# Kernel tuning notes

Measured on AMD Instinct MI355X. Metric: run time of the kernel, lower is better.

## Reference

```python
import jax, jax.numpy as jnp
import numpy as np

B, S, D = 8, 2048, 512
LN_EPS = 1e-5

def _layernorm(x, gamma, beta):
    mu = jnp.mean(x, axis=-1, keepdims=True)
    var = jnp.mean(jnp.square(x - mu), axis=-1, keepdims=True)
    return (x - mu) * jax.lax.rsqrt(var + LN_EPS) * gamma + beta

def setup_inputs() -> dict:
    key = jax.random.key(0)
    ks = jax.random.split(key, 10)
    s_in = 1.0 / np.sqrt(2 * D)
    s_d = 1.0 / np.sqrt(D)
    return {
        "Noise_x": jax.random.normal(ks[0], (B, S, D), jnp.float32),
        "X": jax.random.normal(ks[1], (B, S, D), jnp.float32),
        "cond": jax.random.normal(ks[2], (B, S, D), jnp.float32),
        "W_gate": jax.random.normal(ks[3], (2 * D, D), jnp.float32) * s_in,
        "b_gate": jnp.zeros((D,), jnp.float32),
        "W1": jax.random.normal(ks[4], (D, 2 * D), jnp.float32) * s_d,
        "b1": jnp.zeros((2 * D,), jnp.float32),
        "W2": jax.random.normal(ks[5], (2 * D, D), jnp.float32) * s_in,
        "b2": jnp.zeros((D,), jnp.float32),
        "g1": jnp.ones((D,), jnp.float32),
        "be1": jnp.zeros((D,), jnp.float32),
        "g2": jnp.ones((D,), jnp.float32),
        "be2": jnp.zeros((D,), jnp.float32),
    }

def reference(Noise_x, X, cond, W_gate, b_gate, W1, b1, W2, b2, g1, be1, g2, be2):
    # gated fusion of noise and condition
    combined = jnp.concatenate([Noise_x, cond], axis=-1)            # [B,S,2D]
    gate = jax.nn.sigmoid(combined @ W_gate + b_gate)               # [B,S,D]
    fused = gate * Noise_x + (1.0 - gate) * cond                    # [B,S,D]
    # hand-rolled attention: Q = fused, K = V = X
    scale = 1.0 / jnp.sqrt(jnp.asarray(D, fused.dtype))
    scores = jnp.einsum('bqd,bkd->bqk', fused, X) * scale           # [B,S,S]
    attn = jax.nn.softmax(scores, axis=-1)
    attn_out = jnp.einsum('bqk,bkd->bqd', attn, X)                  # [B,S,D]
    # residual + norm, FFN (exact GELU as in torch default), residual + norm
    q = _layernorm(fused + attn_out, g1, be1)
    ff = jax.nn.gelu(q @ W1 + b1, approximate=False) @ W2 + b2
    return _layernorm(q + ff, g2, be2)
```

## Files before the change

### kernel.cpp

```cpp
#include <hip/hip_runtime.h>
#include <math.h>

typedef unsigned short ushort_t;
typedef unsigned int uint_t;
typedef __attribute__((ext_vector_type(8))) short short8;
typedef __attribute__((ext_vector_type(4))) float floatx4;

constexpr int B = 8;
constexpr int S = 2048;
constexpr int D = 512;
constexpr int BS = B * S;
constexpr float LN_EPS = 1e-5f;
constexpr float ATTN_SCALE = 0.04419417382415922f;


__device__ __forceinline__ ushort_t f2bf(float f) {
    union { float f; uint_t u; } x; x.f = f;
    uint_t r = x.u + 0x7fffu + ((x.u >> 16) & 1u);
    return (ushort_t)(r >> 16);
}
__device__ __forceinline__ float bf2f(ushort_t h) {
    union { uint_t u; float f; } y; y.u = ((uint_t)h) << 16;
    return y.f;
}
__device__ __forceinline__ short8 pack8(float4 a, float4 b) {
    short8 p;
    p[0] = (short)f2bf(a.x); p[1] = (short)f2bf(a.y);
    p[2] = (short)f2bf(a.z); p[3] = (short)f2bf(a.w);
    p[4] = (short)f2bf(b.x); p[5] = (short)f2bf(b.y);
    p[6] = (short)f2bf(b.z); p[7] = (short)f2bf(b.w);
    return p;
}

#define SWZ_DECODE(bx, by, bz)                                                 \
    int bx, by, bz;                                                            \
    {                                                                          \
        const int gx = gridDim.x, gy = gridDim.y;                              \
        const int nwg = gx * gy * (int)gridDim.z;                              \
        const int F = blockIdx.x + gx * (blockIdx.y + gy * blockIdx.z);        \
        const int L = (F & 7) * (nwg >> 3) + (F >> 3);                         \
        bx = L % gx;                                                           \
        const int l2 = L / gx;                                                 \
        by = l2 % gy;                                                          \
        bz = l2 / gy;                                                          \
    }

__device__ __forceinline__ float blk_reduce_sum(float v, float* sm) {
#pragma unroll
    for (int o = 32; o; o >>= 1) v += __shfl_down(v, o, 64);
    __syncthreads();
    if ((threadIdx.x & 63) == 0) sm[threadIdx.x >> 6] = v;
    __syncthreads();
    return sm[0] + sm[1] + sm[2] + sm[3];
}
__device__ __forceinline__ float blk_reduce_max(float v, float* sm) {
#pragma unroll
    for (int o = 32; o; o >>= 1) v = fmaxf(v, __shfl_down(v, o, 64));
    __syncthreads();
    if ((threadIdx.x & 63) == 0) sm[threadIdx.x >> 6] = v;
    __syncthreads();
    return fmaxf(fmaxf(sm[0], sm[1]), fmaxf(sm[2], sm[3]));
}

__global__ __launch_bounds__(256) void transpose_cvt(
    const float* __restrict__ in, ushort_t* __restrict__ out, int R, int C,
    ushort_t* __restrict__ out2) {
    __shared__ float tl[32][33];
    const size_t zoff = (size_t)blockIdx.z * R * C;
    const int tx = threadIdx.x & 31, ty = threadIdx.x >> 5;
    const int c0 = blockIdx.x * 32, r0 = blockIdx.y * 32;
#pragma unroll
    for (int i = 0; i < 4; i++) {
        const float v = in[zoff + (size_t)(r0 + ty + i * 8) * C + c0 + tx];
        tl[ty + i * 8][tx] = v;
        if (out2) out2[zoff + (size_t)(r0 + ty + i * 8) * C + c0 + tx] = f2bf(v);
    }
    __syncthreads();
#pragma unroll
    for (int i = 0; i < 4; i++)
        out[zoff + (size_t)(c0 + ty + i * 8) * R + r0 + tx] = f2bf(tl[tx][ty + i * 8]);
}

#define IDX512()                                                               \
    const int t = threadIdx.x;                                                 \
    const int srow = t >> 2;                                       \
    const int scol = (t & 3) * 8;                               \
    const int lane = t & 63, w = t >> 6;                           \
    const int wm = (w >> 2) * 64, wn = (w & 3) * 32;                           \
    const int fr = lane & 15, fq = lane >> 4;

#define MFMA8W(Asp, Bsp)                                                       \
    {                                                                          \
        short8 af[4], bfg[2];                                                  \
        _Pragma("unroll") for (int i = 0; i < 4; i++)                          \
            af[i]  = *(const short8*)&(Asp)[(wm + i * 16 + fr) * 40 + fq * 8]; \
        _Pragma("unroll") for (int j = 0; j < 2; j++)                          \
            bfg[j] = *(const short8*)&(Bsp)[(wn + j * 16 + fr) * 40 + fq * 8]; \
        _Pragma("unroll") for (int i = 0; i < 4; i++)                          \
            _Pragma("unroll") for (int j = 0; j < 2; j++)                      \
                acc[i][j] = __builtin_amdgcn_mfma_f32_16x16x32_bf16(           \
                    af[i], bfg[j], acc[i][j], 0, 0, 0);                        \
    }

__global__ __launch_bounds__(512) void gate_gemm(
    const float* __restrict__ NX, const float* __restrict__ CD,
    const ushort_t* __restrict__ WgT, const float* __restrict__ bg,
    ushort_t* __restrict__ Fb) {
    __shared__ ushort_t As[2][128 * 40];
    __shared__ ushort_t Bs[2][128 * 40];
    SWZ_DECODE(bx, by, bz);
    (void)bz;
    IDX512();
    const int m0 = by * 128, n0 = bx * 128;
    floatx4 acc[4][2];
#pragma unroll
    for (int i = 0; i < 4; i++)
#pragma unroll
        for (int j = 0; j < 2; j++) {
            acc[i][j][0] = 0.f; acc[i][j][1] = 0.f;
            acc[i][j][2] = 0.f; acc[i][j][3] = 0.f;
        }
    const ushort_t* Bb = WgT + (size_t)n0 * 1024;

    float4 fa0, fa1;
    int4 b0;
    {
        const float* p0 = NX + (size_t)(m0 + srow) * 512 + scol;
        fa0 = *(const float4*)p0;  fa1 = *(const float4*)(p0 + 4);
        b0 = *(const int4*)(Bb + (size_t)srow * 1024 + scol);
        *(short8*)&As[0][srow * 40 + scol] = pack8(fa0, fa1);
        *(int4*)&Bs[0][srow * 40 + scol] = b0;
    }
    {
        const float* p0 = NX + (size_t)(m0 + srow) * 512 + 32 + scol;
        fa0 = *(const float4*)p0;  fa1 = *(const float4*)(p0 + 4);
        b0 = *(const int4*)(Bb + (size_t)srow * 1024 + 32 + scol);
    }
    __syncthreads();

    int cur = 0;
    for (int k0 = 0; k0 < 1024; k0 += 32) {
        MFMA8W(As[cur], Bs[cur]);
        const int kn = k0 + 32;
        if (kn < 1024) {
            *(short8*)&As[cur ^ 1][srow * 40 + scol] = pack8(fa0, fa1);
            *(int4*)&Bs[cur ^ 1][srow * 40 + scol] = b0;
            const int kf = kn + 32;
            if (kf < 1024) {
                const float* Asrc = (kf < 512) ? NX : CD;
                const int kk = kf & 511;
                const float* p0 = Asrc + (size_t)(m0 + srow) * 512 + kk + scol;
                fa0 = *(const float4*)p0;  fa1 = *(const float4*)(p0 + 4);
                b0 = *(const int4*)(Bb + (size_t)srow * 1024 + kf + scol);
            }
        }
        __syncthreads();
        cur ^= 1;
    }

#pragma unroll
    for (int i = 0; i < 4; i++) {
#pragma unroll
        for (int j = 0; j < 2; j++) {
#pragma unroll
            for (int r = 0; r < 4; r++) {
                const int m = m0 + wm + i * 16 + fq * 4 + r;
                const int n = n0 + wn + j * 16 + fr;
                const float z = acc[i][j][r] + bg[n];
                const float g = 1.f / (1.f + expf(-z));
                const size_t idx = (size_t)m * 512 + n;
                Fb[idx] = f2bf(g * NX[idx] + (1.f - g) * CD[idx]);
            }
        }
    }
}

template <int EPI>
__global__ __launch_bounds__(512) void gemm2_std(
    const ushort_t* __restrict__ A, int lda, long sAz,
    const ushort_t* __restrict__ Bt, int ldb, long sBz,
    void* __restrict__ Cv, int ldc, long sCz,
    int K, const float* __restrict__ bias, float scale, int init) {
    __shared__ ushort_t As[2][128 * 40];
    __shared__ ushort_t Bs[2][128 * 40];
    SWZ_DECODE(bx, by, bz);
    IDX512();
    const int m0 = by * 128, n0 = bx * 128;
    floatx4 acc[4][2];
#pragma unroll
    for (int i = 0; i < 4; i++)
#pragma unroll
        for (int j = 0; j < 2; j++) {
            acc[i][j][0] = 0.f; acc[i][j][1] = 0.f;
            acc[i][j][2] = 0.f; acc[i][j][3] = 0.f;
        }
    const ushort_t* Ab = A + (size_t)bz * sAz + (size_t)m0 * lda;
    const ushort_t* Bb = Bt + (size_t)bz * sBz + (size_t)n0 * ldb;

    int4 a0 = *(const int4*)(Ab + (size_t)srow * lda + scol);
    int4 b0 = *(const int4*)(Bb + (size_t)srow * ldb + scol);
    *(int4*)&As[0][srow * 40 + scol] = a0;
    *(int4*)&Bs[0][srow * 40 + scol] = b0;
    if (32 < K) {
        a0 = *(const int4*)(Ab + (size_t)srow * lda + 32 + scol);
        b0 = *(const int4*)(Bb + (size_t)srow * ldb + 32 + scol);
    }
    __syncthreads();

    int cur = 0;
    for (int k0 = 0; k0 < K; k0 += 32) {
        MFMA8W(As[cur], Bs[cur]);
        const int kn = k0 + 32;
        if (kn < K) {
            *(int4*)&As[cur ^ 1][srow * 40 + scol] = a0;
            *(int4*)&Bs[cur ^ 1][srow * 40 + scol] = b0;
            const int kf = kn + 32;
            if (kf < K) {
                a0 = *(const int4*)(Ab + (size_t)srow * lda + kf + scol);
                b0 = *(const int4*)(Bb + (size_t)srow * ldb + kf + scol);
            }
        }
        __syncthreads();
        cur ^= 1;
    }

#pragma unroll
    for (int i = 0; i < 4; i++) {
#pragma unroll
        for (int j = 0; j < 2; j++) {
#pragma unroll
            for (int r = 0; r < 4; r++) {
                const int m = m0 + wm + i * 16 + fq * 4 + r;
                const int n = n0 + wn + j * 16 + fr;
                float v = acc[i][j][r];
                if (EPI == 0) {
                    ushort_t* C = (ushort_t*)Cv + (size_t)bz * sCz;
                    C[(size_t)m * ldc + n] = f2bf(v * scale);
                } else if (EPI == 1) {
                    const float x = v + bias[n];
                    const float gl = 0.5f * x * (1.f + erff(x * 0.70710678118654752f));
                    ushort_t* C = (ushort_t*)Cv;
                    C[(size_t)m * ldc + n] = f2bf(gl);
                } else {
                    float* T = (float*)Cv;
                    const size_t idx = (size_t)m * ldc + n;
                    T[idx] = T[idx] + v + (init ? bias[n] : 0.f);
                }
            }
        }
    }
}

#define IDX128()                                                               \
    const int t = threadIdx.x;                                                 \
    const int sr = t >> 2;                                          \
    const int sc = (t & 3) * 8;                                 \
    const int lane = t & 63, w = t >> 6;                                       \
    const int fr = lane & 15, fq = lane >> 4;

#define MFMA8(Asp, Bsp)                                                        \
    {                                                                          \
        short8 af[2], bfg[4];                                                  \
        _Pragma("unroll") for (int i = 0; i < 2; i++)                          \
            af[i]  = *(const short8*)&(Asp)[(wm + i * 16 + fr) * 40 + fq * 8]; \
        _Pragma("unroll") for (int j = 0; j < 4; j++)                          \
            bfg[j] = *(const short8*)&(Bsp)[(j * 16 + fr) * 40 + fq * 8];      \
        _Pragma("unroll") for (int i = 0; i < 2; i++)                          \
            _Pragma("unroll") for (int j = 0; j < 4; j++)                      \
                acc[i][j] = __builtin_amdgcn_mfma_f32_16x16x32_bf16(           \
                    af[i], bfg[j], acc[i][j], 0, 0, 0);                        \
    }

template <int EPI>
__global__ __launch_bounds__(256) void gemm3_std(
    const ushort_t* __restrict__ A, int lda, long sAz,
    const ushort_t* __restrict__ Bt, int ldb, long sBz,
    void* __restrict__ Cv, int ldc, long sCz,
    int K, const float* __restrict__ bias, float scale, int init) {
    __shared__ ushort_t As[2][128 * 40];
    __shared__ ushort_t Bs[2][64 * 40];
    SWZ_DECODE(bx, by, bz);
    IDX128();
    const int m0 = by * 128, n0 = bx * 64;
    const int wm = w * 32;
    floatx4 acc[2][4];
#pragma unroll
    for (int i = 0; i < 2; i++)
#pragma unroll
        for (int j = 0; j < 4; j++) {
            acc[i][j][0] = 0.f; acc[i][j][1] = 0.f;
            acc[i][j][2] = 0.f; acc[i][j][3] = 0.f;
        }
    const ushort_t* Ab = A + (size_t)bz * sAz + (size_t)m0 * lda;
    const ushort_t* Bb = Bt + (size_t)bz * sBz + (size_t)n0 * ldb;

    int4 a0 = *(const int4*)(Ab + (size_t)sr * lda + sc);
    int4 a1 = *(const int4*)(Ab + (size_t)(sr + 64) * lda + sc);
    int4 b0 = *(const int4*)(Bb + (size_t)sr * ldb + sc);
    *(int4*)&As[0][sr * 40 + sc] = a0;
    *(int4*)&As[0][(sr + 64) * 40 + sc] = a1;
    *(int4*)&Bs[0][sr * 40 + sc] = b0;
    if (32 < K) {
        a0 = *(const int4*)(Ab + (size_t)sr * lda + 32 + sc);
        a1 = *(const int4*)(Ab + (size_t)(sr + 64) * lda + 32 + sc);
        b0 = *(const int4*)(Bb + (size_t)sr * ldb + 32 + sc);
    }
    __syncthreads();

    int cur = 0;
    for (int k0 = 0; k0 < K; k0 += 32) {
        MFMA8(As[cur], Bs[cur]);
        const int kn = k0 + 32;
        if (kn < K) {
            *(int4*)&As[cur ^ 1][sr * 40 + sc] = a0;
            *(int4*)&As[cur ^ 1][(sr + 64) * 40 + sc] = a1;
            *(int4*)&Bs[cur ^ 1][sr * 40 + sc] = b0;
            const int kf = kn + 32;
            if (kf < K) {
                a0 = *(const int4*)(Ab + (size_t)sr * lda + kf + sc);
                a1 = *(const int4*)(Ab + (size_t)(sr + 64) * lda + kf + sc);
                b0 = *(const int4*)(Bb + (size_t)sr * ldb + kf + sc);
            }
        }
        __syncthreads();
        cur ^= 1;
    }

#pragma unroll
    for (int i = 0; i < 2; i++) {
#pragma unroll
        for (int j = 0; j < 4; j++) {
#pragma unroll
            for (int r = 0; r < 4; r++) {
                const int m = m0 + wm + i * 16 + fq * 4 + r;
                const int n = n0 + j * 16 + fr;
                float v = acc[i][j][r];
                if (EPI == 0) {
                    ushort_t* C = (ushort_t*)Cv + (size_t)bz * sCz;
                    C[(size_t)m * ldc + n] = f2bf(v * scale);
                } else if (EPI == 1) {
                    const float x = v + bias[n];
                    const float gl = 0.5f * x * (1.f + erff(x * 0.70710678118654752f));
                    ushort_t* C = (ushort_t*)Cv;
                    C[(size_t)m * ldc + n] = f2bf(gl);
                } else {
                    float* T = (float*)Cv;
                    const size_t idx = (size_t)m * ldc + n;
                    T[idx] = T[idx] + v + (init ? bias[n] : 0.f);
                }
            }
        }
    }
}

__global__ __launch_bounds__(256) void softmax_bf16(ushort_t* __restrict__ Sc) {
    __shared__ float sm[4];
    ushort_t* row = Sc + (size_t)blockIdx.x * 2048;
    const int t = threadIdx.x;
    ushort_t raw[8];
    *(int4*)raw = *(const int4*)(row + t * 8);
    float e[8];
    float mx = -1e30f;
#pragma unroll
    for (int j = 0; j < 8; j++) { e[j] = bf2f(raw[j]); mx = fmaxf(mx, e[j]); }
    mx = blk_reduce_max(mx, sm);
    float s = 0.f;
#pragma unroll
    for (int j = 0; j < 8; j++) { e[j] = expf(e[j] - mx); s += e[j]; }
    s = blk_reduce_sum(s, sm);
    const float inv = 1.f / s;
#pragma unroll
    for (int j = 0; j < 8; j++) raw[j] = f2bf(e[j] * inv);
    *(int4*)(row + t * 8) = *(const int4*)raw;
}

__global__ __launch_bounds__(256) void ln1_kernel(
    const ushort_t* __restrict__ Fb, const ushort_t* __restrict__ Ab,
    const float* __restrict__ g1, const float* __restrict__ be1,
    float* __restrict__ qf, ushort_t* __restrict__ qb) {
    const int l = threadIdx.x & 63, wv = threadIdx.x >> 6;
    const size_t row = (size_t)blockIdx.x * 4 + wv;
    const size_t base = row * 512 + l * 8;
    ushort_t fb[8], ab[8];
    *(int4*)fb = *(const int4*)(Fb + base);
    *(int4*)ab = *(const int4*)(Ab + base);
    float v[8];
    float s = 0.f;
#pragma unroll
    for (int j = 0; j < 8; j++) { v[j] = bf2f(fb[j]) + bf2f(ab[j]); s += v[j]; }
#pragma unroll
    for (int o = 32; o; o >>= 1) s += __shfl_xor(s, o, 64);
    const float mu = s * (1.f / 512.f);
    float vs = 0.f;
#pragma unroll
    for (int j = 0; j < 8; j++) { v[j] -= mu; vs += v[j] * v[j]; }
#pragma unroll
    for (int o = 32; o; o >>= 1) vs += __shfl_xor(vs, o, 64);
    const float rs = rsqrtf(vs * (1.f / 512.f) + LN_EPS);
    const int c = l * 8;
    float4 ga = *(const float4*)(g1 + c),  gb = *(const float4*)(g1 + c + 4);
    float4 ba = *(const float4*)(be1 + c), bb = *(const float4*)(be1 + c + 4);
    float y[8];
    y[0] = v[0] * rs * ga.x + ba.x; y[1] = v[1] * rs * ga.y + ba.y;
    y[2] = v[2] * rs * ga.z + ba.z; y[3] = v[3] * rs * ga.w + ba.w;
    y[4] = v[4] * rs * gb.x + bb.x; y[5] = v[5] * rs * gb.y + bb.y;
    y[6] = v[6] * rs * gb.z + bb.z; y[7] = v[7] * rs * gb.w + bb.w;
    *(float4*)(qf + base)     = make_float4(y[0], y[1], y[2], y[3]);
    *(float4*)(qf + base + 4) = make_float4(y[4], y[5], y[6], y[7]);
    ushort_t qo[8];
#pragma unroll
    for (int j = 0; j < 8; j++) qo[j] = f2bf(y[j]);
    *(int4*)(qb + base) = *(const int4*)qo;
}

__global__ __launch_bounds__(256) void ln2_kernel(
    float* __restrict__ T, const float* __restrict__ g,
    const float* __restrict__ be) {
    const int l = threadIdx.x & 63, wv = threadIdx.x >> 6;
    const size_t row = (size_t)blockIdx.x * 4 + wv;
    const size_t base = row * 512 + l * 8;
    float4 t0 = *(const float4*)(T + base);
    float4 t1 = *(const float4*)(T + base + 4);
    float v[8] = {t0.x, t0.y, t0.z, t0.w, t1.x, t1.y, t1.z, t1.w};
    float s = 0.f;
#pragma unroll
    for (int j = 0; j < 8; j++) s += v[j];
#pragma unroll
    for (int o = 32; o; o >>= 1) s += __shfl_xor(s, o, 64);
    const float mu = s * (1.f / 512.f);
    float vs = 0.f;
#pragma unroll
    for (int j = 0; j < 8; j++) { v[j] -= mu; vs += v[j] * v[j]; }
#pragma unroll
    for (int o = 32; o; o >>= 1) vs += __shfl_xor(vs, o, 64);
    const float rs = rsqrtf(vs * (1.f / 512.f) + LN_EPS);
    const int c = l * 8;
    float4 ga = *(const float4*)(g + c),  gb = *(const float4*)(g + c + 4);
    float4 ba = *(const float4*)(be + c), bb = *(const float4*)(be + c + 4);
    *(float4*)(T + base) = make_float4(
        v[0] * rs * ga.x + ba.x, v[1] * rs * ga.y + ba.y,
        v[2] * rs * ga.z + ba.z, v[3] * rs * ga.w + ba.w);
    *(float4*)(T + base + 4) = make_float4(
        v[4] * rs * gb.x + bb.x, v[5] * rs * gb.y + bb.y,
        v[6] * rs * gb.z + bb.z, v[7] * rs * gb.w + bb.w);
}

extern "C" void kernel_launch(void* const* d_in, const int* in_sizes, int n_in,
                              void* d_out, int out_size, void* d_ws, size_t ws_size,
                              hipStream_t stream) {
    const float* NX  = (const float*)d_in[0];
    const float* X   = (const float*)d_in[1];
    const float* CD  = (const float*)d_in[2];
    const float* Wg  = (const float*)d_in[3];
    const float* bg  = (const float*)d_in[4];
    const float* W1  = (const float*)d_in[5];
    const float* b1  = (const float*)d_in[6];
    const float* W2  = (const float*)d_in[7];
    const float* b2  = (const float*)d_in[8];
    const float* g1  = (const float*)d_in[9];
    const float* be1 = (const float*)d_in[10];
    const float* g2  = (const float*)d_in[11];
    const float* be2 = (const float*)d_in[12];

    ushort_t* slot0 = (ushort_t*)d_ws;
    ushort_t* slot1 = (ushort_t*)((char*)d_ws + 16777216);
    ushort_t* slot2 = (ushort_t*)((char*)d_ws + 33554432);
    ushort_t* Xb    = slot0;
    ushort_t* attnb = slot0;
    ushort_t* hbuf  = slot0;
    ushort_t* Fb    = slot1;
    ushort_t* W1T   = slot1;
    ushort_t* W2T   = slot1 + 524288;
    ushort_t* WgT   = slot2;
    ushort_t* XbT   = slot2;
    ushort_t* qb    = slot2;
    ushort_t* Scb   = (ushort_t*)d_out;
    float*    qf    = (float*)d_out;

    transpose_cvt<<<dim3(512 / 32, 1024 / 32, 1), 256, 0, stream>>>(
        Wg, WgT, 1024, 512, nullptr);

    gate_gemm<<<dim3(4, 128), 512, 0, stream>>>(NX, CD, WgT, bg, Fb);

    transpose_cvt<<<dim3(512 / 32, 2048 / 32, 8), 256, 0, stream>>>(
        X, XbT, 2048, 512, Xb);

    for (int g = 0; g < 2; g++) {
        const size_t go = (size_t)g * 4 * S * 512;
        gemm2_std<0><<<dim3(16, 16, 4), 512, 0, stream>>>(
            Fb + go, D, (long)S * D,
            Xb + go, D, (long)S * D,
            (void*)Scb, S, (long)S * S, D, nullptr, ATTN_SCALE, 0);
        softmax_bf16<<<4 * S, 256, 0, stream>>>(Scb);
        gemm3_std<0><<<dim3(8, 16, 4), 256, 0, stream>>>(
            Scb, S, (long)S * S,
            XbT + go, S, (long)D * S,
            (void*)(attnb + go), 512, (long)S * 512, S, nullptr, 1.f, 0);
    }

    ln1_kernel<<<BS / 4, 256, 0, stream>>>(Fb, attnb, g1, be1, qf, qb);

    transpose_cvt<<<dim3(1024 / 32, 512 / 32, 1), 256, 0, stream>>>(
        W1, W1T, 512, 1024, nullptr);
    transpose_cvt<<<dim3(512 / 32, 1024 / 32, 1), 256, 0, stream>>>(
        W2, W2T, 1024, 512, nullptr);

    for (int h = 0; h < 2; h++) {
        gemm2_std<1><<<dim3(4, 128), 512, 0, stream>>>(
            qb, 512, 0, W1T + (size_t)h * 512 * 512, 512, 0,
            (void*)hbuf, 512, 0, 512, b1 + h * 512, 1.f, 0);
        gemm2_std<2><<<dim3(4, 128), 512, 0, stream>>>(
            hbuf, 512, 0, W2T + h * 512, 1024, 0,
            (void*)qf, 512, 0, 512, b2, 1.f, h == 0 ? 1 : 0);
    }

    ln2_kernel<<<BS / 4, 256, 0, stream>>>(qf, g2, be2);
}
```

Measured before the change: 474.9 us.

## Merge FFN halves into single full-width GEMMs reading fp32 LN output directly

The FFN was split into two halves of the hidden width, each run as a W1 GEMM and an accumulating W2 GEMM. It now uses one ffn1 GEMM over the full 1024-wide hidden layer and one W2 GEMM with K=1024. The new ffn1 kernel reads the fp32 LayerNorm output and converts it to bf16 while staging it into shared memory, so ln1 no longer writes a separate bf16 copy. This cuts kernel launches, avoids the fp32 read-modify-write of qf in the second accumulating pass, and drops one bf16 write. The trade-off is a 32MB hidden buffer and fp32 reads in the first FFN GEMM.

```diff
diff --git a/kernel.cpp b/kernel.cpp
--- a/kernel.cpp
+++ b/kernel.cpp
@@ -102,6 +102,13 @@
                     af[i], bfg[j], acc[i][j], 0, 0, 0);                        \
     }
 
+#define ACC42_INIT()                                                           \
+    floatx4 acc[4][2];                                                         \
+    _Pragma("unroll") for (int i = 0; i < 4; i++)                              \
+        _Pragma("unroll") for (int j = 0; j < 2; j++) {                        \
+            acc[i][j][0] = 0.f; acc[i][j][1] = 0.f;                            \
+            acc[i][j][2] = 0.f; acc[i][j][3] = 0.f; }
+
 __global__ __launch_bounds__(512) void gate_gemm(
     const float* __restrict__ NX, const float* __restrict__ CD,
     const ushort_t* __restrict__ WgT, const float* __restrict__ bg,
@@ -112,14 +119,7 @@
     (void)bz;
     IDX512();
     const int m0 = by * 128, n0 = bx * 128;
-    floatx4 acc[4][2];
-#pragma unroll
-    for (int i = 0; i < 4; i++)
-#pragma unroll
-        for (int j = 0; j < 2; j++) {
-            acc[i][j][0] = 0.f; acc[i][j][1] = 0.f;
-            acc[i][j][2] = 0.f; acc[i][j][3] = 0.f;
-        }
+    ACC42_INIT();
     const ushort_t* Bb = WgT + (size_t)n0 * 1024;
 
     float4 fa0, fa1;
@@ -186,14 +186,7 @@
     SWZ_DECODE(bx, by, bz);
     IDX512();
     const int m0 = by * 128, n0 = bx * 128;
-    floatx4 acc[4][2];
-#pragma unroll
-    for (int i = 0; i < 4; i++)
-#pragma unroll
-        for (int j = 0; j < 2; j++) {
-            acc[i][j][0] = 0.f; acc[i][j][1] = 0.f;
-            acc[i][j][2] = 0.f; acc[i][j][3] = 0.f;
-        }
+    ACC42_INIT();
     const ushort_t* Ab = A + (size_t)bz * sAz + (size_t)m0 * lda;
     const ushort_t* Bb = Bt + (size_t)bz * sBz + (size_t)n0 * ldb;
 
@@ -236,16 +229,73 @@
                 if (EPI == 0) {
                     ushort_t* C = (ushort_t*)Cv + (size_t)bz * sCz;
                     C[(size_t)m * ldc + n] = f2bf(v * scale);
-                } else if (EPI == 1) {
-                    const float x = v + bias[n];
-                    const float gl = 0.5f * x * (1.f + erff(x * 0.70710678118654752f));
-                    ushort_t* C = (ushort_t*)Cv;
-                    C[(size_t)m * ldc + n] = f2bf(gl);
                 } else {
                     float* T = (float*)Cv;
                     const size_t idx = (size_t)m * ldc + n;
                     T[idx] = T[idx] + v + (init ? bias[n] : 0.f);
                 }
+            }
+        }
+    }
+}
+
+__global__ __launch_bounds__(512) void ffn1_gemm(
+    const float* __restrict__ Aq, const ushort_t* __restrict__ W1T,
+    const float* __restrict__ b1, ushort_t* __restrict__ Hid) {
+    __shared__ ushort_t As[2][128 * 40];
+    __shared__ ushort_t Bs[2][128 * 40];
+    SWZ_DECODE(bx, by, bz);
+    (void)bz;
+    IDX512();
+    const int m0 = by * 128, n0 = bx * 128;
+    ACC42_INIT();
+    const ushort_t* Bb = W1T + (size_t)n0 * 512;
+
+    float4 fa0, fa1;
+    int4 b0;
+    {
+        const float* p0 = Aq + (size_t)(m0 + srow) * 512 + scol;
+        fa0 = *(const float4*)p0;  fa1 = *(const float4*)(p0 + 4);
+        b0 = *(const int4*)(Bb + (size_t)srow * 512 + scol);
+        *(short8*)&As[0][srow * 40 + scol] = pack8(fa0, fa1);
+        *(int4*)&Bs[0][srow * 40 + scol] = b0;
+    }
+    {
+        const float* p0 = Aq + (size_t)(m0 + srow) * 512 + 32 + scol;
+        fa0 = *(const float4*)p0;  fa1 = *(const float4*)(p0 + 4);
+        b0 = *(const int4*)(Bb + (size_t)srow * 512 + 32 + scol);
+    }
+    __syncthreads();
+
+    int cur = 0;
+    for (int k0 = 0; k0 < 512; k0 += 32) {
+        MFMA8W(As[cur], Bs[cur]);
+        const int kn = k0 + 32;
+        if (kn < 512) {
+            *(short8*)&As[cur ^ 1][srow * 40 + scol] = pack8(fa0, fa1);
+            *(int4*)&Bs[cur ^ 1][srow * 40 + scol] = b0;
+            const int kf = kn + 32;
+            if (kf < 512) {
+                const float* p0 = Aq + (size_t)(m0 + srow) * 512 + kf + scol;
+                fa0 = *(const float4*)p0;  fa1 = *(const float4*)(p0 + 4);
+                b0 = *(const int4*)(Bb + (size_t)srow * 512 + kf + scol);
+            }
+        }
+        __syncthreads();
+        cur ^= 1;
+    }
+
+#pragma unroll
+    for (int i = 0; i < 4; i++) {
+#pragma unroll
+        for (int j = 0; j < 2; j++) {
+#pragma unroll
+            for (int r = 0; r < 4; r++) {
+                const int m = m0 + wm + i * 16 + fq * 4 + r;
+                const int n = n0 + wn + j * 16 + fr;
+                const float x = acc[i][j][r] + b1[n];
+                const float gl = 0.5f * x * (1.f + erff(x * 0.70710678118654752f));
+                Hid[(size_t)m * 1024 + n] = f2bf(gl);
             }
         }
     }
@@ -271,12 +321,10 @@
                     af[i], bfg[j], acc[i][j], 0, 0, 0);                        \
     }
 
-template <int EPI>
-__global__ __launch_bounds__(256) void gemm3_std(
+__global__ __launch_bounds__(256) void gemm3_pv(
     const ushort_t* __restrict__ A, int lda, long sAz,
     const ushort_t* __restrict__ Bt, int ldb, long sBz,
-    void* __restrict__ Cv, int ldc, long sCz,
-    int K, const float* __restrict__ bias, float scale, int init) {
+    ushort_t* __restrict__ Cb, int ldc, long sCz, int K) {
     __shared__ ushort_t As[2][128 * 40];
     __shared__ ushort_t Bs[2][64 * 40];
     SWZ_DECODE(bx, by, bz);
@@ -334,20 +382,8 @@
             for (int r = 0; r < 4; r++) {
                 const int m = m0 + wm + i * 16 + fq * 4 + r;
                 const int n = n0 + j * 16 + fr;
-                float v = acc[i][j][r];
-                if (EPI == 0) {
-                    ushort_t* C = (ushort_t*)Cv + (size_t)bz * sCz;
-                    C[(size_t)m * ldc + n] = f2bf(v * scale);
-                } else if (EPI == 1) {
-                    const float x = v + bias[n];
-                    const float gl = 0.5f * x * (1.f + erff(x * 0.70710678118654752f));
-                    ushort_t* C = (ushort_t*)Cv;
-                    C[(size_t)m * ldc + n] = f2bf(gl);
-                } else {
-                    float* T = (float*)Cv;
-                    const size_t idx = (size_t)m * ldc + n;
-                    T[idx] = T[idx] + v + (init ? bias[n] : 0.f);
-                }
+                ushort_t* C = Cb + (size_t)bz * sCz;
+                C[(size_t)m * ldc + n] = f2bf(acc[i][j][r]);
             }
         }
     }
@@ -377,7 +413,7 @@
 __global__ __launch_bounds__(256) void ln1_kernel(
     const ushort_t* __restrict__ Fb, const ushort_t* __restrict__ Ab,
     const float* __restrict__ g1, const float* __restrict__ be1,
-    float* __restrict__ qf, ushort_t* __restrict__ qb) {
+    float* __restrict__ qf) {
     const int l = threadIdx.x & 63, wv = threadIdx.x >> 6;
     const size_t row = (size_t)blockIdx.x * 4 + wv;
     const size_t base = row * 512 + l * 8;
@@ -400,17 +436,12 @@
     const int c = l * 8;
     float4 ga = *(const float4*)(g1 + c),  gb = *(const float4*)(g1 + c + 4);
     float4 ba = *(const float4*)(be1 + c), bb = *(const float4*)(be1 + c + 4);
-    float y[8];
-    y[0] = v[0] * rs * ga.x + ba.x; y[1] = v[1] * rs * ga.y + ba.y;
-    y[2] = v[2] * rs * ga.z + ba.z; y[3] = v[3] * rs * ga.w + ba.w;
-    y[4] = v[4] * rs * gb.x + bb.x; y[5] = v[5] * rs * gb.y + bb.y;
-    y[6] = v[6] * rs * gb.z + bb.z; y[7] = v[7] * rs * gb.w + bb.w;
-    *(float4*)(qf + base)     = make_float4(y[0], y[1], y[2], y[3]);
-    *(float4*)(qf + base + 4) = make_float4(y[4], y[5], y[6], y[7]);
-    ushort_t qo[8];
-#pragma unroll
-    for (int j = 0; j < 8; j++) qo[j] = f2bf(y[j]);
-    *(int4*)(qb + base) = *(const int4*)qo;
+    *(float4*)(qf + base) = make_float4(
+        v[0] * rs * ga.x + ba.x, v[1] * rs * ga.y + ba.y,
+        v[2] * rs * ga.z + ba.z, v[3] * rs * ga.w + ba.w);
+    *(float4*)(qf + base + 4) = make_float4(
+        v[4] * rs * gb.x + bb.x, v[5] * rs * gb.y + bb.y,
+        v[6] * rs * gb.z + bb.z, v[7] * rs * gb.w + bb.w);
 }
 
 __global__ __launch_bounds__(256) void ln2_kernel(
@@ -467,13 +498,12 @@
     ushort_t* slot2 = (ushort_t*)((char*)d_ws + 33554432);
     ushort_t* Xb    = slot0;
     ushort_t* attnb = slot0;
-    ushort_t* hbuf  = slot0;
+    ushort_t* hid   = slot0;
     ushort_t* Fb    = slot1;
-    ushort_t* W1T   = slot1;
-    ushort_t* W2T   = slot1 + 524288;
     ushort_t* WgT   = slot2;
     ushort_t* XbT   = slot2;
-    ushort_t* qb    = slot2;
+    ushort_t* W1T   = slot2;
+    ushort_t* W2T   = slot2 + 524288;
     ushort_t* Scb   = (ushort_t*)d_out;
     float*    qf    = (float*)d_out;
 
@@ -492,27 +522,23 @@
             Xb + go, D, (long)S * D,
             (void*)Scb, S, (long)S * S, D, nullptr, ATTN_SCALE, 0);
         softmax_bf16<<<4 * S, 256, 0, stream>>>(Scb);
-        gemm3_std<0><<<dim3(8, 16, 4), 256, 0, stream>>>(
+        gemm3_pv<<<dim3(8, 16, 4), 256, 0, stream>>>(
             Scb, S, (long)S * S,
             XbT + go, S, (long)D * S,
-            (void*)(attnb + go), 512, (long)S * 512, S, nullptr, 1.f, 0);
-    }
-
-    ln1_kernel<<<BS / 4, 256, 0, stream>>>(Fb, attnb, g1, be1, qf, qb);
+            attnb + go, 512, (long)S * 512, S);
+    }
+
+    ln1_kernel<<<BS / 4, 256, 0, stream>>>(Fb, attnb, g1, be1, qf);
 
     transpose_cvt<<<dim3(1024 / 32, 512 / 32, 1), 256, 0, stream>>>(
         W1, W1T, 512, 1024, nullptr);
     transpose_cvt<<<dim3(512 / 32, 1024 / 32, 1), 256, 0, stream>>>(
         W2, W2T, 1024, 512, nullptr);
 
-    for (int h = 0; h < 2; h++) {
-        gemm2_std<1><<<dim3(4, 128), 512, 0, stream>>>(
-            qb, 512, 0, W1T + (size_t)h * 512 * 512, 512, 0,
-            (void*)hbuf, 512, 0, 512, b1 + h * 512, 1.f, 0);
-        gemm2_std<2><<<dim3(4, 128), 512, 0, stream>>>(
-            hbuf, 512, 0, W2T + h * 512, 1024, 0,
-            (void*)qf, 512, 0, 512, b2, 1.f, h == 0 ? 1 : 0);
-    }
+    ffn1_gemm<<<dim3(8, 128), 512, 0, stream>>>(qf, W1T, b1, hid);
+    gemm2_std<2><<<dim3(4, 128), 512, 0, stream>>>(
+        hid, 1024, 0, W2T, 1024, 0,
+        (void*)qf, 512, 0, 1024, b2, 1.f, 1);
 
     ln2_kernel<<<BS / 4, 256, 0, stream>>>(qf, g2, be2);
 }
```

New measurement: 451.0 us. 1.05x faster.
